# Performance work log

Hardware: AMD Instinct MI355X
Metric: run time of the kernel (lower is better)

The kernel has to match this reference:

```python
import jax, jax.numpy as jnp
import numpy as np

EPS = 1e-6
N_HEAD, N_KV_HEAD = 16, 4
VE_GATE_CH = 12

def rmsnorm(x):
    return x * jax.lax.rsqrt(jnp.mean(x * x, axis=-1, keepdims=True) + EPS)

def apply_rotary_emb(x, cos, sin):
    half = x.shape[-1] // 2
    x1, x2 = x[..., :half], x[..., half:]
    return jnp.concatenate([x1 * cos + x2 * sin, -x1 * sin + x2 * cos], axis=-1)

def setup_inputs():
    key = jax.random.key(0)
    ks = jax.random.split(key, 8)
    B, S, D = 2, 2048, 1024
    H, KVH = N_HEAD, N_KV_HEAD
    hd = D // H
    x = jax.random.normal(ks[0], (B, S, D), jnp.float32)
    ve = jax.random.normal(ks[1], (B, S, KVH * hd), jnp.float32)
    # real rotary tables, broadcastable over [B,S,H,hd//2]
    inv_freq = 1.0 / (10000.0 ** (np.arange(hd // 2, dtype=np.float32) / (hd // 2)))
    ang = np.arange(S, dtype=np.float32)[:, None] * inv_freq[None, :]  # [S, hd//2]
    cos = jnp.asarray(np.cos(ang))[:, None, :]  # [S,1,hd//2]
    sin = jnp.asarray(np.sin(ang))[:, None, :]
    std = 0.02
    Wq = jax.random.normal(ks[2], (D, H * hd), jnp.float32) * std
    Wk = jax.random.normal(ks[3], (D, KVH * hd), jnp.float32) * std
    Wv = jax.random.normal(ks[4], (D, KVH * hd), jnp.float32) * std
    Wo = jax.random.normal(ks[5], (D, D), jnp.float32) * std
    Wg = jax.random.normal(ks[6], (VE_GATE_CH, KVH), jnp.float32) * std
    return {"x": x, "ve": ve, "cos": cos, "sin": sin, "Wq": Wq, "Wk": Wk,
            "Wv": Wv, "Wo": Wo, "Wg": Wg, "window_size": 512}

def reference(x, ve, cos, sin, Wq, Wk, Wv, Wo, Wg, window_size):
    B, S, D = x.shape
    H, KVH = N_HEAD, N_KV_HEAD
    hd = D // H
    q = (x @ Wq).reshape(B, S, H, hd)
    k = (x @ Wk).reshape(B, S, KVH, hd)
    v = (x @ Wv).reshape(B, S, KVH, hd)
    # value-embedding gating
    gate = 3.0 * jax.nn.sigmoid(x[..., :VE_GATE_CH] @ Wg)  # [B,S,KVH]
    v = v + gate[..., None] * ve.reshape(B, S, KVH, hd)
    # RoPE + QK rmsnorm * 1.2
    q = rmsnorm(apply_rotary_emb(q, cos, sin)) * 1.2
    k = rmsnorm(apply_rotary_emb(k, cos, sin)) * 1.2
    # GQA head repeat (repeat_interleave over head dim)
    rep = H // KVH
    k = jnp.repeat(k, rep, axis=2)  # [B,S,H,hd]
    v = jnp.repeat(v, rep, axis=2)
    scale = 1.0 / np.sqrt(hd).astype(np.float32)
    scores = jnp.einsum('bqhd,bkhd->bhqk', q, k) * scale  # [B,H,S,S]
    pos = jnp.arange(S)
    allow = (pos[None, :] <= pos[:, None]) & (pos[None, :] >= pos[:, None] - window_size + 1)
    scores = jnp.where(allow[None, None], scores, -jnp.inf)
    attn = jax.nn.softmax(scores, axis=-1)
    y = jnp.einsum('bhqk,bkhd->bqhd', attn, v).reshape(B, S, D)
    return y @ Wo
```

## Files before the change

kernel.cpp:

```cpp
#include <hip/hip_runtime.h>
#include <hip/hip_bf16.h>
#include <cstddef>
#include <cstdint>


typedef short v8s __attribute__((ext_vector_type(8)));
typedef float v4f __attribute__((ext_vector_type(4)));

__device__ __forceinline__ ushort b1(float a) {
  uint u = __float_as_uint(a);
  return (ushort)((u + 0x7FFFu + ((u >> 16) & 1u)) >> 16);
}
__device__ __forceinline__ uint bpack(float lo, float hi) {
  uint ul = __float_as_uint(lo), uh = __float_as_uint(hi);
  ul = (ul + 0x7FFFu + ((ul >> 16) & 1u)) >> 16;
  uh = (uh + 0x7FFFu + ((uh >> 16) & 1u)) & 0xFFFF0000u;
  return ul | uh;
}

__device__ __forceinline__ void async16(const ushort* g, ushort* l) {
  __builtin_amdgcn_global_load_lds(
      (__attribute__((address_space(1))) void*)(uintptr_t)(const void*)g,
      (__attribute__((address_space(3))) void*)(uintptr_t)(void*)l, 16, 0, 0);
}

__global__ __launch_bounds__(256) void prep_all(
    const float* __restrict__ x, ushort* __restrict__ xb,
    const float* __restrict__ Wg, float* __restrict__ gates,
    const float* __restrict__ cosp, const float* __restrict__ sinp,
    float2* __restrict__ cs,
    const float* __restrict__ Wq, const float* __restrict__ Wk,
    const float* __restrict__ Wv, const float* __restrict__ Wo,
    ushort* __restrict__ Wqt, ushort* __restrict__ Wkt,
    ushort* __restrict__ Wvt, ushort* __restrict__ Wot)
{
  const int bx = blockIdx.x, t = threadIdx.x;
  if (bx < 4096) {
    const float* row = x + (size_t)bx * 1024;
    float4 v = *(const float4*)(row + t * 4);
    ushort4 o;
    o.x = b1(v.x); o.y = b1(v.y); o.z = b1(v.z); o.w = b1(v.w);
    *(ushort4*)(xb + (size_t)bx * 1024 + t * 4) = o;
    if (t < 4) {
      float g = 0.f;
#pragma unroll
      for (int i = 0; i < 12; ++i) g += row[i] * Wg[i * 4 + t];
      gates[bx * 4 + t] = 3.0f / (1.0f + __expf(-g));
    }
    return;
  }
  if (bx < 4352) {
    const int i = (bx - 4096) * 256 + t;
    cs[i] = make_float2(cosp[i], sinp[i]);
    return;
  }
  __shared__ ushort tile[32][33];
  int u = bx - 4352;
  const float* W; ushort* Wt; int N, xx, yy;
  if (u < 1024)      { W = Wq; Wt = Wqt; N = 1024; xx = u & 31; yy = u >> 5; }
  else if (u < 2048) { u -= 1024; W = Wo; Wt = Wot; N = 1024; xx = u & 31; yy = u >> 5; }
  else if (u < 2304) { u -= 2048; W = Wk; Wt = Wkt; N = 256;  xx = u & 7;  yy = u >> 3; }
  else               { u -= 2304; W = Wv; Wt = Wvt; N = 256;  xx = u & 7;  yy = u >> 3; }
  const int n0 = xx * 32, k0 = yy * 32;
  const int tx = t & 31, ty = t >> 5;
#pragma unroll
  for (int i = 0; i < 4; ++i) {
    const int k = ty + i * 8;
    tile[k][tx] = b1(W[(size_t)(k0 + k) * N + n0 + tx]);
  }
  __syncthreads();
#pragma unroll
  for (int i = 0; i < 4; ++i) {
    const int n = ty + i * 8;
    Wt[(size_t)(n0 + n) * 1024 + k0 + tx] = tile[tx][n];
  }
}

__device__ __forceinline__ void gemm_mainloop(
    const ushort* __restrict__ A, const ushort* __restrict__ Bt,
    int K, int m0, int n0, ushort (*As)[64], ushort (*Bs)[64],
    v4f acc[4][4])
{
  const int t = threadIdx.x;
  const int lane = t & 63, wave = t >> 6;
  const int wr = wave >> 1, wc = wave & 1;
  const int quad = lane >> 4, l16 = lane & 15;
  const int l8 = lane >> 3, c8 = (lane & 7) * 8;

  const ushort* ap[4];
  const ushort* bp[4];
  ushort* al[4];
  ushort* bl[4];
#pragma unroll
  for (int i = 0; i < 4; ++i) {
    const int row = (wave * 4 + i) * 8 + l8;
    ap[i] = A  + (size_t)(m0 + row) * K + c8;
    bp[i] = Bt + (size_t)(n0 + row) * K + c8;
    al[i] = &As[(wave * 4 + i) * 8][0];
    bl[i] = &Bs[(wave * 4 + i) * 8][0];
  }

  for (int k0 = 0; k0 < K; k0 += 64) {
#pragma unroll
    for (int i = 0; i < 4; ++i) {
      async16(ap[i] + k0, al[i]);
      async16(bp[i] + k0, bl[i]);
    }
    __syncthreads();
#pragma unroll
    for (int ks = 0; ks < 2; ++ks) {
      v8s af[4], bf[4];
#pragma unroll
      for (int i = 0; i < 4; ++i) {
        af[i] = *(const v8s*)&As[wr * 64 + i * 16 + l16][ks * 32 + quad * 8];
        bf[i] = *(const v8s*)&Bs[wc * 64 + i * 16 + l16][ks * 32 + quad * 8];
      }
#pragma unroll
      for (int mt = 0; mt < 4; ++mt)
#pragma unroll
        for (int nt = 0; nt < 4; ++nt)
          acc[mt][nt] = __builtin_amdgcn_mfma_f32_16x16x32_bf16(
              af[mt], bf[nt], acc[mt][nt], 0, 0, 0);
    }
    __syncthreads();
  }
}

__global__ __launch_bounds__(256) void gemm_qkv_fused(
    const ushort* __restrict__ A, const ushort* __restrict__ Bt,
    const float2* __restrict__ cs, const float* __restrict__ gates,
    const float* __restrict__ ve,
    ushort* __restrict__ qb, ushort* __restrict__ kb, ushort* __restrict__ vb)
{
  __shared__ ushort As[128][64];
  __shared__ ushort Bs[128][64];
  const int m0 = blockIdx.x * 128, n0 = blockIdx.y * 128;
  const int lane = threadIdx.x & 63, wave = threadIdx.x >> 6;
  const int wr = wave >> 1, wc = wave & 1;
  const int quad = lane >> 4, l16 = lane & 15;

  v4f acc[4][4];
#pragma unroll
  for (int i = 0; i < 4; ++i)
#pragma unroll
    for (int j = 0; j < 4; ++j) acc[i][j] = (v4f){0.f, 0.f, 0.f, 0.f};

  gemm_mainloop(A, Bt, 1024, m0, n0, As, Bs, acc);

  const int sec = blockIdx.y;
  const int head_col = n0 + wc * 64;

  if (sec < 10) {
    const bool isQ = (sec < 8);
    const int h = (head_col - (isQ ? 0 : 1024)) >> 6;
    ushort* dst = isQ ? qb : kb;
    const int ld = isQ ? 1024 : 256;
#pragma unroll
    for (int mt = 0; mt < 4; ++mt)
#pragma unroll
      for (int r = 0; r < 4; ++r) {
        const int row = m0 + wr * 64 + mt * 16 + quad * 4 + r;
        const int s = row & 2047;
        const float2 cs0 = cs[s * 32 + l16];
        const float2 cs1 = cs[s * 32 + 16 + l16];
        const float x10 = acc[mt][0][r], x11 = acc[mt][1][r];
        const float x20 = acc[mt][2][r], x21 = acc[mt][3][r];
        float ss = x10 * x10 + x11 * x11 + x20 * x20 + x21 * x21;
        ss += __shfl_xor(ss, 1);
        ss += __shfl_xor(ss, 2);
        ss += __shfl_xor(ss, 4);
        ss += __shfl_xor(ss, 8);
        const float rs = rsqrtf(ss * (1.0f / 64.0f) + 1e-6f) * 1.2f;
        ushort* dp = dst + (size_t)row * ld + h * 64 + l16;
        dp[0]  = b1((x10 * cs0.x + x20 * cs0.y) * rs);
        dp[16] = b1((x11 * cs1.x + x21 * cs1.y) * rs);
        dp[32] = b1((-x10 * cs0.y + x20 * cs0.x) * rs);
        dp[48] = b1((-x11 * cs1.y + x21 * cs1.x) * rs);
      }
  } else {
    const int kvh = (head_col - 1280) >> 6;
#pragma unroll
    for (int mt = 0; mt < 4; ++mt)
#pragma unroll
      for (int r = 0; r < 4; ++r) {
        const int row = m0 + wr * 64 + mt * 16 + quad * 4 + r;
        const float gate = gates[row * 4 + kvh];
        const float* vep = ve + (size_t)row * 256 + kvh * 64 + l16;
        ushort* dp = vb + (size_t)row * 256 + kvh * 64 + l16;
#pragma unroll
        for (int nt = 0; nt < 4; ++nt)
          dp[nt * 16] = b1(acc[mt][nt][r] + gate * vep[nt * 16]);
      }
  }
}

__global__ __launch_bounds__(256) void gemm_wo(
    const ushort* __restrict__ A, const ushort* __restrict__ Bt,
    float* __restrict__ C)
{
  __shared__ ushort As[128][64];
  __shared__ ushort Bs[128][64];
  const int m0 = blockIdx.x * 128, n0 = blockIdx.y * 128;
  const int lane = threadIdx.x & 63, wave = threadIdx.x >> 6;
  const int wr = wave >> 1, wc = wave & 1;
  const int quad = lane >> 4, l16 = lane & 15;

  v4f acc[4][4];
#pragma unroll
  for (int i = 0; i < 4; ++i)
#pragma unroll
    for (int j = 0; j < 4; ++j) acc[i][j] = (v4f){0.f, 0.f, 0.f, 0.f};

  gemm_mainloop(A, Bt, 1024, m0, n0, As, Bs, acc);

#pragma unroll
  for (int mt = 0; mt < 4; ++mt)
#pragma unroll
    for (int r = 0; r < 4; ++r) {
      float* cp = C + (size_t)(m0 + wr * 64 + mt * 16 + quad * 4 + r) * 1024
                    + n0 + wc * 64 + l16;
#pragma unroll
      for (int nt = 0; nt < 4; ++nt) cp[nt * 16] = acc[mt][nt][r];
    }
}

__global__ __launch_bounds__(256) void transpose_v(
    const ushort* __restrict__ vb, ushort* __restrict__ vtb)
{
  __shared__ ushort L[64][72];
  const int s0 = blockIdx.x * 64, kvh = blockIdx.y, b = blockIdx.z;
  const int t = threadIdx.x;
#pragma unroll
  for (int i = 0; i < 2; ++i) {
    const int cc = t + i * 256;
    const int srow = cc >> 3, c8 = (cc & 7) * 8;
    *(int4*)&L[srow][c8] =
        *(const int4*)(vb + ((size_t)(b * 2048 + s0 + srow)) * 256 + kvh * 64 + c8);
  }
  __syncthreads();
#pragma unroll
  for (int i = 0; i < 2; ++i) {
    const int cc = t + i * 256;
    const int drow = cc >> 3, s8 = (cc & 7) * 8;
    ushort w[8];
#pragma unroll
    for (int jj = 0; jj < 8; ++jj) w[jj] = L[s8 + jj][drow];
    *(int4*)(vtb + ((size_t)((b * 4 + kvh) * 64 + drow)) * 2048 + s0 + s8) =
        *(int4*)w;
  }
}

__global__ __launch_bounds__(256) void attn_mfma(
    const ushort* __restrict__ qb, const ushort* __restrict__ kb,
    const ushort* __restrict__ vtb, ushort* __restrict__ yb,
    const int* __restrict__ wptr)
{
  __shared__ ushort Ks[64][72];
  __shared__ ushort Vt[80][72];
  __shared__ ushort Ps[128][72];
  const int qt = blockIdx.x, h = blockIdx.y, b = blockIdx.z;
  const int kvh = h >> 2, q0 = qt * 128;
  const int t = threadIdx.x, lane = t & 63, wave = t >> 6;
  const int quad = lane >> 4, l16 = lane & 15;
  const int Wwin = *wptr;

  v8s qf[2][2];
#pragma unroll
  for (int s = 0; s < 2; ++s) {
    const ushort* qp = qb + ((size_t)(b * 2048 + q0 + wave * 32 + s * 16 + l16)) * 1024
                          + h * 64 + quad * 8;
    qf[s][0] = *(const v8s*)qp;
    qf[s][1] = *(const v8s*)(qp + 32);
  }

  if (t < 128) {
    const int row = 64 + (t >> 3), c8 = (t & 7) * 8;
    const int v = (row == 64) ? 0x3F803F80 : 0;
    int4 w; w.x = v; w.y = v; w.z = v; w.w = v;
    *(int4*)&Vt[row][c8] = w;
  }

  v4f o[2][5];
#pragma unroll
  for (int s = 0; s < 2; ++s)
#pragma unroll
    for (int d = 0; d < 5; ++d) o[s][d] = (v4f){0.f, 0.f, 0.f, 0.f};

  const int lo = q0 - Wwin + 1;
  const int kt0 = (lo > 0) ? (lo >> 6) : 0;
  const int kt1 = (q0 + 127) >> 6;

  for (int kt = kt0; kt <= kt1; ++kt) {
#pragma unroll
    for (int i = 0; i < 2; ++i) {
      const int cc = t + i * 256;
      const int r8 = cc >> 3, c8 = (cc & 7) * 8;
      *(int4*)&Ks[r8][c8] =
          *(const int4*)(kb + ((size_t)(b * 2048 + kt * 64 + r8)) * 256 + kvh * 64 + c8);
      *(int4*)&Vt[r8][c8] =
          *(const int4*)(vtb + ((size_t)((b * 4 + kvh) * 64 + r8)) * 2048 + kt * 64 + c8);
    }
    __syncthreads();

    const bool needs_mask = (kt * 64 + 63 > q0) || (kt * 64 < q0 + 128 - Wwin);

#pragma unroll
    for (int s = 0; s < 2; ++s) {
      const int qrow = q0 + wave * 32 + s * 16 + l16;
      ushort* prow = &Ps[wave * 32 + s * 16 + l16][0];
#pragma unroll
      for (int nt = 0; nt < 4; ++nt) {
        v8s kf0 = *(const v8s*)&Ks[nt * 16 + l16][quad * 8];
        v8s kf1 = *(const v8s*)&Ks[nt * 16 + l16][32 + quad * 8];
        v4f st = (v4f){0.f, 0.f, 0.f, 0.f};
        st = __builtin_amdgcn_mfma_f32_16x16x32_bf16(kf0, qf[s][0], st, 0, 0, 0);
        st = __builtin_amdgcn_mfma_f32_16x16x32_bf16(kf1, qf[s][1], st, 0, 0, 0);
        float p[4];
#pragma unroll
        for (int r = 0; r < 4; ++r) {
          p[r] = exp2f(fmaf(st[r], 0.18033688011f, -17.31234049107f));
          if (needs_mask) {
            const int k = kt * 64 + nt * 16 + quad * 4 + r;
            const bool ok = (k <= qrow) && (k > qrow - Wwin);
            p[r] = ok ? p[r] : 0.0f;
          }
        }
        uint2 w;
        w.x = bpack(p[0], p[1]);
        w.y = bpack(p[2], p[3]);
        *(uint2*)(prow + nt * 16 + quad * 4) = w;
      }
    }

    v8s pf[2][2];
#pragma unroll
    for (int s = 0; s < 2; ++s) {
      pf[s][0] = *(const v8s*)&Ps[wave * 32 + s * 16 + l16][quad * 8];
      pf[s][1] = *(const v8s*)&Ps[wave * 32 + s * 16 + l16][32 + quad * 8];
    }
#pragma unroll
    for (int dt = 0; dt < 5; ++dt) {
      v8s vf0 = *(const v8s*)&Vt[dt * 16 + l16][quad * 8];
      v8s vf1 = *(const v8s*)&Vt[dt * 16 + l16][32 + quad * 8];
#pragma unroll
      for (int s = 0; s < 2; ++s) {
        o[s][dt] = __builtin_amdgcn_mfma_f32_16x16x32_bf16(pf[s][0], vf0, o[s][dt], 0, 0, 0);
        o[s][dt] = __builtin_amdgcn_mfma_f32_16x16x32_bf16(pf[s][1], vf1, o[s][dt], 0, 0, 0);
      }
    }
    __syncthreads();
  }

#pragma unroll
  for (int s = 0; s < 2; ++s)
#pragma unroll
    for (int r = 0; r < 4; ++r) {
      const float l = __shfl(o[s][4][r], lane & 48);
      const float inv = 1.0f / l;
      ushort* yp = yb + ((size_t)(b * 2048 + q0 + wave * 32 + s * 16 + quad * 4 + r)) * 1024
                      + h * 64 + l16;
#pragma unroll
      for (int dt = 0; dt < 4; ++dt) yp[dt * 16] = b1(o[s][dt][r] * inv);
    }
}

extern "C" void kernel_launch(void* const* d_in, const int* in_sizes, int n_in,
                              void* d_out, int out_size, void* d_ws, size_t ws_size,
                              hipStream_t stream)
{
  const float* x    = (const float*)d_in[0];
  const float* ve   = (const float*)d_in[1];
  const float* cosp = (const float*)d_in[2];
  const float* sinp = (const float*)d_in[3];
  const float* Wq   = (const float*)d_in[4];
  const float* Wk   = (const float*)d_in[5];
  const float* Wv   = (const float*)d_in[6];
  const float* Wo   = (const float*)d_in[7];
  const float* Wg   = (const float*)d_in[8];
  const int*   win  = (const int*)d_in[9];
  float* out = (float*)d_out;

  char* p = (char*)d_ws;
  ushort* xb    = (ushort*)p;  p += (size_t)4194304 * 2;
  ushort* qb    = (ushort*)p;  p += (size_t)4194304 * 2;
  ushort* yb    = (ushort*)p;  p += (size_t)4194304 * 2;
  ushort* kb    = (ushort*)p;  p += (size_t)1048576 * 2;
  ushort* vb    = (ushort*)p;  p += (size_t)1048576 * 2;
  ushort* vtb   = (ushort*)p;  p += (size_t)1048576 * 2;
  ushort* Wqkvt = (ushort*)p;  p += (size_t)1536 * 1024 * 2;
  ushort* Wot   = (ushort*)p;  p += (size_t)1048576 * 2;
  float2* cs    = (float2*)p;  p += (size_t)65536 * 8;
  float*  gates = (float*)p;

  prep_all<<<6912, 256, 0, stream>>>(
      x, xb, Wg, gates, cosp, sinp, cs, Wq, Wk, Wv, Wo,
      Wqkvt, Wqkvt + (size_t)1024 * 1024, Wqkvt + (size_t)1280 * 1024, Wot);

  gemm_qkv_fused<<<dim3(32, 12), 256, 0, stream>>>(xb, Wqkvt, cs, gates, ve,
                                                   qb, kb, vb);
  transpose_v<<<dim3(32, 4, 2), 256, 0, stream>>>(vb, vtb);

  attn_mfma<<<dim3(16, 16, 2), 256, 0, stream>>>(qb, kb, vtb, yb, win);

  gemm_wo<<<dim3(32, 8), 256, 0, stream>>>(yb, Wot, out);
}
```

Measured before the change: 174.5 us.

## Shrink GEMM M-tile to 64 and fuse V transpose into QKV epilogue

Both GEMMs now use 64x128 tiles, doubling grid size (768 and 512 blocks) so the 256 CUs are better filled. The V-section epilogue writes gated V into shared memory transposed, then stores it straight into the [b,kvh,d,s] layout. This removes the separate transpose_v kernel and its round trip through a vb buffer. In exchange, each tile reuses less data per k-step and there is an extra barrier in the V epilogue.

```diff
diff --git a/kernel.cpp b/kernel.cpp
--- a/kernel.cpp
+++ b/kernel.cpp
@@ -76,10 +76,10 @@
   }
 }
 
-__device__ __forceinline__ void gemm_mainloop(
+__device__ __forceinline__ void gemm_mainloop64(
     const ushort* __restrict__ A, const ushort* __restrict__ Bt,
     int K, int m0, int n0, ushort (*As)[64], ushort (*Bs)[64],
-    v4f acc[4][4])
+    v4f acc[2][4])
 {
   const int t = threadIdx.x;
   const int lane = t & 63, wave = t >> 6;
@@ -87,36 +87,38 @@
   const int quad = lane >> 4, l16 = lane & 15;
   const int l8 = lane >> 3, c8 = (lane & 7) * 8;
 
-  const ushort* ap[4];
-  const ushort* bp[4];
-  ushort* al[4];
-  ushort* bl[4];
+  const ushort* ap[2]; ushort* al[2];
+  const ushort* bp[4]; ushort* bl[4];
+#pragma unroll
+  for (int i = 0; i < 2; ++i) {
+    const int row = wave * 16 + i * 8;
+    ap[i] = A + (size_t)(m0 + row + l8) * K + c8;
+    al[i] = &As[row][0];
+  }
 #pragma unroll
   for (int i = 0; i < 4; ++i) {
-    const int row = (wave * 4 + i) * 8 + l8;
-    ap[i] = A  + (size_t)(m0 + row) * K + c8;
-    bp[i] = Bt + (size_t)(n0 + row) * K + c8;
-    al[i] = &As[(wave * 4 + i) * 8][0];
-    bl[i] = &Bs[(wave * 4 + i) * 8][0];
+    const int row = wave * 32 + i * 8;
+    bp[i] = Bt + (size_t)(n0 + row + l8) * K + c8;
+    bl[i] = &Bs[row][0];
   }
 
   for (int k0 = 0; k0 < K; k0 += 64) {
 #pragma unroll
-    for (int i = 0; i < 4; ++i) {
-      async16(ap[i] + k0, al[i]);
-      async16(bp[i] + k0, bl[i]);
-    }
+    for (int i = 0; i < 2; ++i) async16(ap[i] + k0, al[i]);
+#pragma unroll
+    for (int i = 0; i < 4; ++i) async16(bp[i] + k0, bl[i]);
     __syncthreads();
 #pragma unroll
     for (int ks = 0; ks < 2; ++ks) {
-      v8s af[4], bf[4];
-#pragma unroll
-      for (int i = 0; i < 4; ++i) {
-        af[i] = *(const v8s*)&As[wr * 64 + i * 16 + l16][ks * 32 + quad * 8];
+      v8s af[2], bf[4];
+#pragma unroll
+      for (int i = 0; i < 2; ++i)
+        af[i] = *(const v8s*)&As[wr * 32 + i * 16 + l16][ks * 32 + quad * 8];
+#pragma unroll
+      for (int i = 0; i < 4; ++i)
         bf[i] = *(const v8s*)&Bs[wc * 64 + i * 16 + l16][ks * 32 + quad * 8];
-      }
-#pragma unroll
-      for (int mt = 0; mt < 4; ++mt)
+#pragma unroll
+      for (int mt = 0; mt < 2; ++mt)
 #pragma unroll
         for (int nt = 0; nt < 4; ++nt)
           acc[mt][nt] = __builtin_amdgcn_mfma_f32_16x16x32_bf16(
@@ -130,36 +132,37 @@
     const ushort* __restrict__ A, const ushort* __restrict__ Bt,
     const float2* __restrict__ cs, const float* __restrict__ gates,
     const float* __restrict__ ve,
-    ushort* __restrict__ qb, ushort* __restrict__ kb, ushort* __restrict__ vb)
-{
-  __shared__ ushort As[128][64];
+    ushort* __restrict__ qb, ushort* __restrict__ kb, ushort* __restrict__ vtb)
+{
+  __shared__ ushort As[64][64];
   __shared__ ushort Bs[128][64];
-  const int m0 = blockIdx.x * 128, n0 = blockIdx.y * 128;
-  const int lane = threadIdx.x & 63, wave = threadIdx.x >> 6;
+  const int m0 = blockIdx.x * 64, n0 = blockIdx.y * 128;
+  const int t = threadIdx.x;
+  const int lane = t & 63, wave = t >> 6;
   const int wr = wave >> 1, wc = wave & 1;
   const int quad = lane >> 4, l16 = lane & 15;
 
-  v4f acc[4][4];
-#pragma unroll
-  for (int i = 0; i < 4; ++i)
+  v4f acc[2][4];
+#pragma unroll
+  for (int i = 0; i < 2; ++i)
 #pragma unroll
     for (int j = 0; j < 4; ++j) acc[i][j] = (v4f){0.f, 0.f, 0.f, 0.f};
 
-  gemm_mainloop(A, Bt, 1024, m0, n0, As, Bs, acc);
+  gemm_mainloop64(A, Bt, 1024, m0, n0, As, Bs, acc);
 
   const int sec = blockIdx.y;
-  const int head_col = n0 + wc * 64;
 
   if (sec < 10) {
     const bool isQ = (sec < 8);
+    const int head_col = n0 + wc * 64;
     const int h = (head_col - (isQ ? 0 : 1024)) >> 6;
     ushort* dst = isQ ? qb : kb;
     const int ld = isQ ? 1024 : 256;
 #pragma unroll
-    for (int mt = 0; mt < 4; ++mt)
+    for (int mt = 0; mt < 2; ++mt)
 #pragma unroll
       for (int r = 0; r < 4; ++r) {
-        const int row = m0 + wr * 64 + mt * 16 + quad * 4 + r;
+        const int row = m0 + wr * 32 + mt * 16 + quad * 4 + r;
         const int s = row & 2047;
         const float2 cs0 = cs[s * 32 + l16];
         const float2 cs1 = cs[s * 32 + 16 + l16];
@@ -178,19 +181,31 @@
         dp[48] = b1((-x11 * cs1.y + x21 * cs1.x) * rs);
       }
   } else {
-    const int kvh = (head_col - 1280) >> 6;
-#pragma unroll
-    for (int mt = 0; mt < 4; ++mt)
+    const int kvh0 = (sec - 10) * 2;
+    const int kvh = kvh0 + wc;
+#pragma unroll
+    for (int mt = 0; mt < 2; ++mt)
 #pragma unroll
       for (int r = 0; r < 4; ++r) {
-        const int row = m0 + wr * 64 + mt * 16 + quad * 4 + r;
+        const int lm = wr * 32 + mt * 16 + quad * 4 + r;
+        const int row = m0 + lm;
         const float gate = gates[row * 4 + kvh];
-        const float* vep = ve + (size_t)row * 256 + kvh * 64 + l16;
-        ushort* dp = vb + (size_t)row * 256 + kvh * 64 + l16;
+        const float* vep = ve + (size_t)row * 256 + kvh * 64;
 #pragma unroll
         for (int nt = 0; nt < 4; ++nt)
-          dp[nt * 16] = b1(acc[mt][nt][r] + gate * vep[nt * 16]);
+          Bs[wc * 64 + nt * 16 + l16][lm] =
+              b1(acc[mt][nt][r] + gate * vep[nt * 16 + l16]);
       }
+    __syncthreads();
+    const int b = m0 >> 11, s0 = m0 & 2047;
+#pragma unroll
+    for (int i = 0; i < 4; ++i) {
+      const int u = t + i * 256;
+      const int lc = u >> 3, seg = u & 7;
+      const int d = lc & 63, kh = kvh0 + (lc >> 6);
+      *(int4*)(vtb + ((size_t)((b * 4 + kh) * 64 + d)) * 2048 + s0 + seg * 8) =
+          *(const int4*)&Bs[lc][seg * 8];
+    }
   }
 }
 
@@ -198,56 +213,30 @@
     const ushort* __restrict__ A, const ushort* __restrict__ Bt,
     float* __restrict__ C)
 {
-  __shared__ ushort As[128][64];
+  __shared__ ushort As[64][64];
   __shared__ ushort Bs[128][64];
-  const int m0 = blockIdx.x * 128, n0 = blockIdx.y * 128;
+  const int m0 = blockIdx.x * 64, n0 = blockIdx.y * 128;
   const int lane = threadIdx.x & 63, wave = threadIdx.x >> 6;
   const int wr = wave >> 1, wc = wave & 1;
   const int quad = lane >> 4, l16 = lane & 15;
 
-  v4f acc[4][4];
-#pragma unroll
-  for (int i = 0; i < 4; ++i)
+  v4f acc[2][4];
+#pragma unroll
+  for (int i = 0; i < 2; ++i)
 #pragma unroll
     for (int j = 0; j < 4; ++j) acc[i][j] = (v4f){0.f, 0.f, 0.f, 0.f};
 
-  gemm_mainloop(A, Bt, 1024, m0, n0, As, Bs, acc);
-
-#pragma unroll
-  for (int mt = 0; mt < 4; ++mt)
+  gemm_mainloop64(A, Bt, 1024, m0, n0, As, Bs, acc);
+
+#pragma unroll
+  for (int mt = 0; mt < 2; ++mt)
 #pragma unroll
     for (int r = 0; r < 4; ++r) {
-      float* cp = C + (size_t)(m0 + wr * 64 + mt * 16 + quad * 4 + r) * 1024
+      float* cp = C + (size_t)(m0 + wr * 32 + mt * 16 + quad * 4 + r) * 1024
                     + n0 + wc * 64 + l16;
 #pragma unroll
       for (int nt = 0; nt < 4; ++nt) cp[nt * 16] = acc[mt][nt][r];
     }
-}
-
-__global__ __launch_bounds__(256) void transpose_v(
-    const ushort* __restrict__ vb, ushort* __restrict__ vtb)
-{
-  __shared__ ushort L[64][72];
-  const int s0 = blockIdx.x * 64, kvh = blockIdx.y, b = blockIdx.z;
-  const int t = threadIdx.x;
-#pragma unroll
-  for (int i = 0; i < 2; ++i) {
-    const int cc = t + i * 256;
-    const int srow = cc >> 3, c8 = (cc & 7) * 8;
-    *(int4*)&L[srow][c8] =
-        *(const int4*)(vb + ((size_t)(b * 2048 + s0 + srow)) * 256 + kvh * 64 + c8);
-  }
-  __syncthreads();
-#pragma unroll
-  for (int i = 0; i < 2; ++i) {
-    const int cc = t + i * 256;
-    const int drow = cc >> 3, s8 = (cc & 7) * 8;
-    ushort w[8];
-#pragma unroll
-    for (int jj = 0; jj < 8; ++jj) w[jj] = L[s8 + jj][drow];
-    *(int4*)(vtb + ((size_t)((b * 4 + kvh) * 64 + drow)) * 2048 + s0 + s8) =
-        *(int4*)w;
-  }
 }
 
 __global__ __launch_bounds__(256) void attn_mfma(
@@ -385,7 +374,6 @@
   ushort* qb    = (ushort*)p;  p += (size_t)4194304 * 2;
   ushort* yb    = (ushort*)p;  p += (size_t)4194304 * 2;
   ushort* kb    = (ushort*)p;  p += (size_t)1048576 * 2;
-  ushort* vb    = (ushort*)p;  p += (size_t)1048576 * 2;
   ushort* vtb   = (ushort*)p;  p += (size_t)1048576 * 2;
   ushort* Wqkvt = (ushort*)p;  p += (size_t)1536 * 1024 * 2;
   ushort* Wot   = (ushort*)p;  p += (size_t)1048576 * 2;
@@ -396,11 +384,10 @@
       x, xb, Wg, gates, cosp, sinp, cs, Wq, Wk, Wv, Wo,
       Wqkvt, Wqkvt + (size_t)1024 * 1024, Wqkvt + (size_t)1280 * 1024, Wot);
 
-  gemm_qkv_fused<<<dim3(32, 12), 256, 0, stream>>>(xb, Wqkvt, cs, gates, ve,
-                                                   qb, kb, vb);
-  transpose_v<<<dim3(32, 4, 2), 256, 0, stream>>>(vb, vtb);
+  gemm_qkv_fused<<<dim3(64, 12), 256, 0, stream>>>(xb, Wqkvt, cs, gates, ve,
+                                                   qb, kb, vtb);
 
   attn_mfma<<<dim3(16, 16, 2), 256, 0, stream>>>(qb, kb, vtb, yb, win);
 
-  gemm_wo<<<dim3(32, 8), 256, 0, stream>>>(yb, Wot, out);
-}
+  gemm_wo<<<dim3(64, 8), 256, 0, stream>>>(yb, Wot, out);
+}
```

New measurement: 179.6 us. 1.03x slower.
